# Kernel tuning notes

Measured on AMD Instinct MI355X. Metric: run time of the kernel, lower is better.

## Reference

```python
import jax, jax.numpy as jnp
import numpy as np

CLASSES = 128
M_IN = 64
N_OUT = 32
N_SAMPLES = 65536


def setup_inputs() -> dict:
    key = jax.random.key(0)
    k1, k2, k3, k4 = jax.random.split(key, 4)
    x = jax.random.normal(k1, (N_SAMPLES, M_IN), dtype=jnp.float32)
    inds = jax.random.randint(k2, (N_SAMPLES,), 0, CLASSES, dtype=jnp.int64)
    # Conv2d(in=M_IN, out=CLASSES*N_OUT, kernel=1) -> weight (CLASSES*N_OUT, M_IN), bias (CLASSES*N_OUT,)
    bound = 1.0 / np.sqrt(M_IN)
    W = jax.random.uniform(k3, (CLASSES * N_OUT, M_IN), minval=-bound, maxval=bound, dtype=jnp.float32)
    b = jax.random.uniform(k4, (CLASSES * N_OUT,), minval=-bound, maxval=bound, dtype=jnp.float32)
    return {"x": x, "inds": inds, "W": W, "b": b}


def reference(x, inds, W, b):
    # 1x1 conv == GEMM: (N, m) @ (m, classes*n) + bias -> (N, classes*n)
    y = jnp.einsum("nm,cm->nc", x, W) + b  # (N, classes*n_out)
    y = y.reshape(-1, CLASSES, N_OUT)       # (N, classes, n_out)
    # gather the selected class slice per sample
    idx = inds.astype(jnp.int32)[:, None, None]  # (N, 1, 1)
    out = jnp.take_along_axis(y, jnp.broadcast_to(idx, (y.shape[0], 1, N_OUT)), axis=1)
    return out.reshape(-1, N_OUT)
```

## Files before the change

kernel.cpp:

```cpp
#include <hip/hip_runtime.h>

#define CLASSES    128
#define M_IN       64
#define N_OUT      32
#define N_SAMPLES  65536
#define BUCKET_CAP N_SAMPLES

typedef __attribute__((ext_vector_type(8))) short bf16x8;
typedef __attribute__((ext_vector_type(4))) float f32x4;

__device__ inline short f2bf(float f) {
    unsigned u = __builtin_bit_cast(unsigned, f);
    u += 0x7fffu + ((u >> 16) & 1u);
    return (short)(u >> 16);
}

__device__ inline bf16x8 cvt8(const float4 a, const float4 b) {
    bf16x8 r;
    r[0] = f2bf(a.x); r[1] = f2bf(a.y); r[2] = f2bf(a.z); r[3] = f2bf(a.w);
    r[4] = f2bf(b.x); r[5] = f2bf(b.y); r[6] = f2bf(b.z); r[7] = f2bf(b.w);
    return r;
}

__global__ __launch_bounds__(256) void scatter_kernel(
    const int* __restrict__ inds,
    int*       __restrict__ cnt,
    int*       __restrict__ bucket)
{
    __shared__ int lcnt[CLASSES];
    __shared__ int lbase[CLASSES];
    const int tid = threadIdx.x;
    if (tid < CLASSES) lcnt[tid] = 0;
    __syncthreads();

    const int  vi = blockIdx.x * 256 + tid;
    const int2 cc = reinterpret_cast<const int2*>(inds)[vi];
    const int  i0 = vi * 2, i1 = i0 + 1;
    const int  p0 = atomicAdd(&lcnt[cc.x], 1);
    const int  p1 = atomicAdd(&lcnt[cc.y], 1);
    __syncthreads();

    if (tid < CLASSES) lbase[tid] = atomicAdd(&cnt[tid], lcnt[tid]);
    __syncthreads();

    bucket[cc.x * BUCKET_CAP + lbase[cc.x] + p0] = i0;
    bucket[cc.y * BUCKET_CAP + lbase[cc.y] + p1] = i1;
}

__global__ __launch_bounds__(256) void compute_kernel(
    const float* __restrict__ x,
    const float* __restrict__ W,
    const float* __restrict__ b,
    const int*   __restrict__ cnt,
    const int*   __restrict__ bucket,
    float*       __restrict__ out)
{
    const int c    = blockIdx.x >> 2;
    const int j4   = blockIdx.x & 3;
    const int wv   = threadIdx.x >> 6;
    const int lane = threadIdx.x & 63;
    const int m16  = lane & 15;
    const int quad = lane >> 4;

    const int  cn = cnt[c];
    const int* bk = bucket + c * BUCKET_CAP;

    bf16x8 Bf[2][2];
#pragma unroll
    for (int nh = 0; nh < 2; ++nh)
#pragma unroll
        for (int kh = 0; kh < 2; ++kh) {
            const float* p = W + (size_t)(c * N_OUT + nh * 16 + m16) * M_IN
                               + kh * 32 + quad * 8;
            Bf[nh][kh] = cvt8(*(const float4*)p, *(const float4*)(p + 4));
        }
    const float b0 = b[c * N_OUT + m16];
    const float b1 = b[c * N_OUT + 16 + m16];

    if (cn == 0) return;
    const int T = (cn + 15) >> 4;
    int t = j4 * 4 + wv;
    if (t >= T) return;

    int base = t << 4;
    {
    }
    int pa = base + m16;
    int na = bk[(pa < cn) ? pa : (cn - 1)];
    const float* xr = x + (size_t)na * M_IN + quad * 8;
    float4 xa0 = *(const float4*)xr,        xa1 = *(const float4*)(xr + 4);
    float4 xa2 = *(const float4*)(xr + 32), xa3 = *(const float4*)(xr + 36);

    while (true) {
        const int  tn   = t + 16;
        const bool more = tn < T;

        int base_n = base, na_n = na;
        float4 xb0 = xa0, xb1 = xa1, xb2 = xa2, xb3 = xa3;
        if (more) {
            base_n = tn << 4;
            const int pan = base_n + m16;
            na_n = bk[(pan < cn) ? pan : (cn - 1)];
            const float* xrn = x + (size_t)na_n * M_IN + quad * 8;
            xb0 = *(const float4*)xrn;        xb1 = *(const float4*)(xrn + 4);
            xb2 = *(const float4*)(xrn + 32); xb3 = *(const float4*)(xrn + 36);
        }

        const bf16x8 A0 = cvt8(xa0, xa1);
        const bf16x8 A1 = cvt8(xa2, xa3);
        f32x4 acc0 = {0.f, 0.f, 0.f, 0.f};
        f32x4 acc1 = {0.f, 0.f, 0.f, 0.f};
        acc0 = __builtin_amdgcn_mfma_f32_16x16x32_bf16(A0, Bf[0][0], acc0, 0, 0, 0);
        acc0 = __builtin_amdgcn_mfma_f32_16x16x32_bf16(A1, Bf[0][1], acc0, 0, 0, 0);
        acc1 = __builtin_amdgcn_mfma_f32_16x16x32_bf16(A0, Bf[1][0], acc1, 0, 0, 0);
        acc1 = __builtin_amdgcn_mfma_f32_16x16x32_bf16(A1, Bf[1][1], acc1, 0, 0, 0);

#pragma unroll
        for (int r = 0; r < 4; ++r) {
            const int p = base + quad * 4 + r;
            if (p < cn) {
                const int n = bk[p];
                out[(size_t)n * N_OUT + m16]      = acc0[r] + b0;
                out[(size_t)n * N_OUT + 16 + m16] = acc1[r] + b1;
            }
        }

        if (!more) break;
        t = tn; base = base_n; na = na_n;
        xa0 = xb0; xa1 = xb1; xa2 = xb2; xa3 = xb3;
    }
}

extern "C" void kernel_launch(void* const* d_in, const int* in_sizes, int n_in,
                              void* d_out, int out_size, void* d_ws, size_t ws_size,
                              hipStream_t stream) {
    const float* x    = (const float*)d_in[0];
    const int*   inds = (const int*)  d_in[1];
    const float* W    = (const float*)d_in[2];
    const float* b    = (const float*)d_in[3];
    float*       out  = (float*)d_out;

    int* cnt    = (int*)d_ws;
    int* bucket = (int*)d_ws + 1024;

    hipMemsetAsync(cnt, 0, CLASSES * sizeof(int), stream);
    scatter_kernel<<<N_SAMPLES / 512, 256, 0, stream>>>(inds, cnt, bucket);
    compute_kernel<<<CLASSES * 4, 256, 0, stream>>>(x, W, b, cnt, bucket, out);
}
```

Measured before the change: 80.91 us.

## Fuse class bucketing and grouped GEMM into one cooperative kernel with grid sync

Merges the scatter kernel and the compute kernel into one cooperatively launched kernel. Each of the 512 blocks buckets 128 sample indices, then all blocks meet at a grid-wide barrier before the per-class MFMA GEMM. The W loads are issued before the scatter so their latency overlaps with it. This removes one kernel launch and the gap between launches, at the cost of a grid barrier and a cooperative-launch requirement that all 512 blocks be resident at once.

```diff
diff --git a/kernel.cpp b/kernel.cpp
--- a/kernel.cpp
+++ b/kernel.cpp
@@ -1,4 +1,7 @@
 #include <hip/hip_runtime.h>
+#include <hip/hip_cooperative_groups.h>
+
+namespace cg = cooperative_groups;
 
 #define CLASSES    128
 #define M_IN       64
@@ -22,69 +25,69 @@
     return r;
 }
 
-__global__ __launch_bounds__(256) void scatter_kernel(
-    const int* __restrict__ inds,
-    int*       __restrict__ cnt,
-    int*       __restrict__ bucket)
-{
-    __shared__ int lcnt[CLASSES];
-    __shared__ int lbase[CLASSES];
-    const int tid = threadIdx.x;
-    if (tid < CLASSES) lcnt[tid] = 0;
-    __syncthreads();
-
-    const int  vi = blockIdx.x * 256 + tid;
-    const int2 cc = reinterpret_cast<const int2*>(inds)[vi];
-    const int  i0 = vi * 2, i1 = i0 + 1;
-    const int  p0 = atomicAdd(&lcnt[cc.x], 1);
-    const int  p1 = atomicAdd(&lcnt[cc.y], 1);
-    __syncthreads();
-
-    if (tid < CLASSES) lbase[tid] = atomicAdd(&cnt[tid], lcnt[tid]);
-    __syncthreads();
-
-    bucket[cc.x * BUCKET_CAP + lbase[cc.x] + p0] = i0;
-    bucket[cc.y * BUCKET_CAP + lbase[cc.y] + p1] = i1;
-}
-
-__global__ __launch_bounds__(256) void compute_kernel(
+__global__ __launch_bounds__(256) void fused_kernel(
     const float* __restrict__ x,
+    const int*   __restrict__ inds,
     const float* __restrict__ W,
     const float* __restrict__ b,
-    const int*   __restrict__ cnt,
-    const int*   __restrict__ bucket,
+    int*         __restrict__ cnt,
+    int*         __restrict__ bucket,
     float*       __restrict__ out)
 {
+    const int tid  = threadIdx.x;
     const int c    = blockIdx.x >> 2;
     const int j4   = blockIdx.x & 3;
-    const int wv   = threadIdx.x >> 6;
-    const int lane = threadIdx.x & 63;
+    const int wv   = tid >> 6;
+    const int lane = tid & 63;
     const int m16  = lane & 15;
     const int quad = lane >> 4;
 
-    const int  cn = cnt[c];
-    const int* bk = bucket + c * BUCKET_CAP;
-
-    bf16x8 Bf[2][2];
+    float4 braw[2][2][2];
 #pragma unroll
     for (int nh = 0; nh < 2; ++nh)
 #pragma unroll
         for (int kh = 0; kh < 2; ++kh) {
             const float* p = W + (size_t)(c * N_OUT + nh * 16 + m16) * M_IN
                                + kh * 32 + quad * 8;
-            Bf[nh][kh] = cvt8(*(const float4*)p, *(const float4*)(p + 4));
+            braw[nh][kh][0] = *(const float4*)p;
+            braw[nh][kh][1] = *(const float4*)(p + 4);
         }
     const float b0 = b[c * N_OUT + m16];
     const float b1 = b[c * N_OUT + 16 + m16];
 
+    __shared__ int lcnt[CLASSES];
+    __shared__ int lbase[CLASSES];
+    if (tid < CLASSES) lcnt[tid] = 0;
+    __syncthreads();
+
+    int i_s = 0, c_s = 0, p_s = 0;
+    if (tid < 128) {
+        i_s = blockIdx.x * 128 + tid;
+        c_s = inds[i_s];
+        p_s = atomicAdd(&lcnt[c_s], 1);
+    }
+    __syncthreads();
+    if (tid < CLASSES) lbase[tid] = atomicAdd(&cnt[tid], lcnt[tid]);
+    __syncthreads();
+    if (tid < 128) bucket[c_s * BUCKET_CAP + lbase[c_s] + p_s] = i_s;
+
+    bf16x8 Bf[2][2];
+#pragma unroll
+    for (int nh = 0; nh < 2; ++nh)
+#pragma unroll
+        for (int kh = 0; kh < 2; ++kh)
+            Bf[nh][kh] = cvt8(braw[nh][kh][0], braw[nh][kh][1]);
+
+    cg::this_grid().sync();
+
+    const int cn = cnt[c];
     if (cn == 0) return;
+    const int* bk = bucket + c * BUCKET_CAP;
     const int T = (cn + 15) >> 4;
     int t = j4 * 4 + wv;
     if (t >= T) return;
 
     int base = t << 4;
-    {
-    }
     int pa = base + m16;
     int na = bk[(pa < cn) ? pa : (cn - 1)];
     const float* xr = x + (size_t)na * M_IN + quad * 8;
@@ -137,13 +140,16 @@
     const float* x    = (const float*)d_in[0];
     const int*   inds = (const int*)  d_in[1];
     const float* W    = (const float*)d_in[2];
-    const float* b    = (const float*)d_in[3];
+    const float* bia  = (const float*)d_in[3];
     float*       out  = (float*)d_out;
 
     int* cnt    = (int*)d_ws;
     int* bucket = (int*)d_ws + 1024;
 
     hipMemsetAsync(cnt, 0, CLASSES * sizeof(int), stream);
-    scatter_kernel<<<N_SAMPLES / 512, 256, 0, stream>>>(inds, cnt, bucket);
-    compute_kernel<<<CLASSES * 4, 256, 0, stream>>>(x, W, b, cnt, bucket, out);
+
+    void* args[] = {(void*)&x, (void*)&inds, (void*)&W, (void*)&bia,
+                    (void*)&cnt, (void*)&bucket, (void*)&out};
+    hipLaunchCooperativeKernel(reinterpret_cast<void*>(fused_kernel),
+                               dim3(CLASSES * 4), dim3(256), args, 0, stream);
 }
```

After: 142.9 us. 76.6% more time.
